# Kernel tuning notes

Hardware: AMD Instinct MI355X
Metric: run time of the kernel (lower is better)

## Reference

```python
import jax, jax.numpy as jnp
import numpy as np


def setup_inputs() -> dict:
    key = jax.random.key(0)
    ks = jax.random.split(key, 7)
    B, T, C, H = 8, 2048, 2048, 128
    x = jax.random.normal(ks[0], (B, T, C), dtype=jnp.float32)
    Wq = jax.random.normal(ks[1], (C, H), dtype=jnp.float32) * (C ** -0.5)
    bq = jax.random.normal(ks[2], (H,), dtype=jnp.float32) * 0.02
    Wk = jax.random.normal(ks[3], (C, H), dtype=jnp.float32) * (C ** -0.5)
    bk = jax.random.normal(ks[4], (H,), dtype=jnp.float32) * 0.02
    Wv = jax.random.normal(ks[5], (C, H), dtype=jnp.float32) * (C ** -0.5)
    bv = jax.random.normal(ks[6], (H,), dtype=jnp.float32) * 0.02
    return {"x": x, "Wq": Wq, "bq": bq, "Wk": Wk, "bk": bk, "Wv": Wv, "bv": bv}


def reference(x, Wq, bq, Wk, bk, Wv, bv):
    # Single-head causal self-attention (dropout in eval mode = identity).
    B, T, C = x.shape
    H = Wq.shape[1]
    Q = jnp.einsum("btc,ch->bth", x, Wq) + bq  # [B,T,H]
    K = jnp.einsum("btc,ch->bth", x, Wk) + bk
    V = jnp.einsum("btc,ch->bth", x, Wv) + bv
    scale = H ** -0.5
    wei = jnp.einsum("bth,bsh->bts", Q, K) * scale  # [B,T,T]
    causal = jnp.tril(jnp.ones((T, T), dtype=bool))
    wei = jnp.where(causal, wei, -jnp.inf)
    wei = jax.nn.softmax(wei, axis=-1)
    out = jnp.einsum("bts,bsh->bth", wei, V)  # [B,T,H]
    return out
```

## Files before the change

kernel.cpp:

```cpp
#include <hip/hip_runtime.h>

typedef float f32x4 __attribute__((ext_vector_type(4)));
typedef short short8 __attribute__((ext_vector_type(8)));
typedef unsigned short ushort8 __attribute__((ext_vector_type(8)));

#define AS1 __attribute__((address_space(1)))
#define AS3 __attribute__((address_space(3)))

#define WS_Q  786432
#define WS_K  2883584
#define WS_VT 4980736

__device__ __forceinline__ unsigned short f2bf(float x) {
    unsigned u = __float_as_uint(x);
    u += 0x7FFFu + ((u >> 16) & 1u);
    return (unsigned short)(u >> 16);
}

__device__ __forceinline__ short8 cvt8(float4 lo, float4 hi) {
    union { unsigned u[4]; short8 s; } r;
    asm("v_cvt_pk_bf16_f32 %0, %1, %2" : "=v"(r.u[0]) : "v"(lo.x), "v"(lo.y));
    asm("v_cvt_pk_bf16_f32 %0, %1, %2" : "=v"(r.u[1]) : "v"(lo.z), "v"(lo.w));
    asm("v_cvt_pk_bf16_f32 %0, %1, %2" : "=v"(r.u[2]) : "v"(hi.x), "v"(hi.y));
    asm("v_cvt_pk_bf16_f32 %0, %1, %2" : "=v"(r.u[3]) : "v"(hi.z), "v"(hi.w));
    return r.s;
}

__device__ __forceinline__ int swz128(int row, int cbyte) {
    return row * 128 + (cbyte ^ ((row & 7) << 4));
}

__global__ __launch_bounds__(256) void wt_kernel(const float* __restrict__ Wq,
        const float* __restrict__ Wk, const float* __restrict__ Wv,
        unsigned short* __restrict__ ws) {
    __shared__ __align__(16) unsigned short tile[64][136];
    int mat = blockIdx.x >> 5, ct = blockIdx.x & 31;
    const float* W = (mat == 0) ? Wq : ((mat == 1) ? Wk : Wv);
    int cbase = ct * 64;
    int tid = threadIdx.x;
#pragma unroll
    for (int p = 0; p < 8; p++) {
        int fidx = p * 256 + tid;
        int row = fidx >> 5;
        int c4 = (fidx & 31) << 2;
        float4 v = *(const float4*)&W[(size_t)(cbase + row) * 128 + c4];
        tile[row][c4 + 0] = f2bf(v.x);
        tile[row][c4 + 1] = f2bf(v.y);
        tile[row][c4 + 2] = f2bf(v.z);
        tile[row][c4 + 3] = f2bf(v.w);
    }
    __syncthreads();
    int h = tid >> 1, seg = tid & 1;
    unsigned short* base = ws + mat * 262144 + ct * 8192 + h * 64;
#pragma unroll
    for (int q4 = 0; q4 < 4; q4++) {
        ushort8 pk;
#pragma unroll
        for (int e = 0; e < 8; e++) pk[e] = tile[seg * 32 + q4 * 8 + e][h];
        int g = seg * 4 + q4;
        *(ushort8*)(base + ((g ^ (h & 7)) << 3)) = pk;
    }
}

__global__ __launch_bounds__(256, 3) void qkv_kernel(const float* __restrict__ x,
        const float* __restrict__ bq, const float* __restrict__ bk,
        const float* __restrict__ bv, unsigned short* __restrict__ ws) {
    __shared__ __align__(16) char lds[2][24576];
    int bid = blockIdx.x;
    int g = bid / 24, j = bid - g * 24;
    int matrix = j >> 3;
    int mt = g * 8 + (j & 7);
    const unsigned short* WTt = ws + matrix * 262144;
    const float* x0 = x + (size_t)mt * 64 * 2048;
    int tid = threadIdx.x, lane = tid & 63, wid = tid >> 6;
    int lr = lane & 15, lg = lane >> 4;
    int m0 = (wid >> 1) * 32, n0 = (wid & 1) * 64;

    int rowA = tid >> 2, qa = tid & 3;
    const float* aSrc = x0 + (size_t)rowA * 2048 + qa * 16;
    int aD0 = rowA * 128 + ((((qa * 2 + 0)) ^ (rowA & 7)) << 4);
    int aD1 = rowA * 128 + ((((qa * 2 + 1)) ^ (rowA & 7)) << 4);

    int aOff00, aOff01, aOff10, aOff11;
    int bOff00, bOff01, bOff10, bOff11, bOff20, bOff21, bOff30, bOff31;
    {
        int r0 = m0 + lr, r1 = m0 + 16 + lr;
        aOff00 = r0 * 128 + (((0 * 4 + lg) ^ (r0 & 7)) << 4);
        aOff01 = r0 * 128 + (((1 * 4 + lg) ^ (r0 & 7)) << 4);
        aOff10 = r1 * 128 + (((0 * 4 + lg) ^ (r1 & 7)) << 4);
        aOff11 = r1 * 128 + (((1 * 4 + lg) ^ (r1 & 7)) << 4);
        int h0 = n0 + lr, h1 = n0 + 16 + lr, h2 = n0 + 32 + lr, h3 = n0 + 48 + lr;
        bOff00 = 8192 + h0 * 128 + (((0 * 4 + lg) ^ (h0 & 7)) << 4);
        bOff01 = 8192 + h0 * 128 + (((1 * 4 + lg) ^ (h0 & 7)) << 4);
        bOff10 = 8192 + h1 * 128 + (((0 * 4 + lg) ^ (h1 & 7)) << 4);
        bOff11 = 8192 + h1 * 128 + (((1 * 4 + lg) ^ (h1 & 7)) << 4);
        bOff20 = 8192 + h2 * 128 + (((0 * 4 + lg) ^ (h2 & 7)) << 4);
        bOff21 = 8192 + h2 * 128 + (((1 * 4 + lg) ^ (h2 & 7)) << 4);
        bOff30 = 8192 + h3 * 128 + (((0 * 4 + lg) ^ (h3 & 7)) << 4);
        bOff31 = 8192 + h3 * 128 + (((1 * 4 + lg) ^ (h3 & 7)) << 4);
    }

    f32x4 acc[2][4];
#pragma unroll
    for (int i = 0; i < 2; i++)
#pragma unroll
        for (int j3 = 0; j3 < 4; j3++) acc[i][j3] = (f32x4){0.f, 0.f, 0.f, 0.f};
    float4 rA0, rA1, rA2, rA3;

#define ISSUE_AB(BUF, T) do { \
        const float* ap_ = aSrc + (size_t)(T) * 64; \
        rA0 = *(const float4*)ap_;        rA1 = *(const float4*)(ap_ + 4); \
        rA2 = *(const float4*)(ap_ + 8);  rA3 = *(const float4*)(ap_ + 12); \
        const unsigned short* bs_ = WTt + (size_t)(T) * 8192 + tid * 8; \
        char* bd_ = &lds[BUF][8192] + tid * 16; \
        __builtin_amdgcn_global_load_lds((const AS1 unsigned*)(bs_), \
            (AS3 unsigned*)(bd_), 16, 0, 0); \
        __builtin_amdgcn_global_load_lds((const AS1 unsigned*)(bs_ + 2048), \
            (AS3 unsigned*)(bd_ + 4096), 16, 0, 0); \
        __builtin_amdgcn_global_load_lds((const AS1 unsigned*)(bs_ + 4096), \
            (AS3 unsigned*)(bd_ + 8192), 16, 0, 0); \
        __builtin_amdgcn_global_load_lds((const AS1 unsigned*)(bs_ + 6144), \
            (AS3 unsigned*)(bd_ + 12288), 16, 0, 0); \
    } while (0)
#define WRITE_A(BUF) do { \
        short8 p0_ = cvt8(rA0, rA1); \
        short8 p1_ = cvt8(rA2, rA3); \
        *(short8*)(&lds[BUF][0] + aD0) = p0_; \
        *(short8*)(&lds[BUF][0] + aD1) = p1_; \
    } while (0)

#define QKV_BODY(T, CUR, STAGE, BAR) do { \
        if (STAGE) ISSUE_AB((CUR) ^ 1, (T) + 1); \
        const char* Lb_ = &lds[CUR][0]; \
        short8 a00 = *(const short8*)(Lb_ + aOff00); \
        short8 a01 = *(const short8*)(Lb_ + aOff01); \
        short8 a10 = *(const short8*)(Lb_ + aOff10); \
        short8 a11 = *(const short8*)(Lb_ + aOff11); \
        short8 b00 = *(const short8*)(Lb_ + bOff00); \
        short8 b01 = *(const short8*)(Lb_ + bOff01); \
        short8 b10 = *(const short8*)(Lb_ + bOff10); \
        short8 b11 = *(const short8*)(Lb_ + bOff11); \
        short8 b20 = *(const short8*)(Lb_ + bOff20); \
        short8 b21 = *(const short8*)(Lb_ + bOff21); \
        short8 b30 = *(const short8*)(Lb_ + bOff30); \
        short8 b31 = *(const short8*)(Lb_ + bOff31); \
        __builtin_amdgcn_s_setprio(1); \
        acc[0][0] = __builtin_amdgcn_mfma_f32_16x16x32_bf16(a00, b00, acc[0][0], 0, 0, 0); \
        acc[0][1] = __builtin_amdgcn_mfma_f32_16x16x32_bf16(a00, b10, acc[0][1], 0, 0, 0); \
        acc[0][2] = __builtin_amdgcn_mfma_f32_16x16x32_bf16(a00, b20, acc[0][2], 0, 0, 0); \
        acc[0][3] = __builtin_amdgcn_mfma_f32_16x16x32_bf16(a00, b30, acc[0][3], 0, 0, 0); \
        acc[1][0] = __builtin_amdgcn_mfma_f32_16x16x32_bf16(a10, b00, acc[1][0], 0, 0, 0); \
        acc[1][1] = __builtin_amdgcn_mfma_f32_16x16x32_bf16(a10, b10, acc[1][1], 0, 0, 0); \
        acc[1][2] = __builtin_amdgcn_mfma_f32_16x16x32_bf16(a10, b20, acc[1][2], 0, 0, 0); \
        acc[1][3] = __builtin_amdgcn_mfma_f32_16x16x32_bf16(a10, b30, acc[1][3], 0, 0, 0); \
        acc[0][0] = __builtin_amdgcn_mfma_f32_16x16x32_bf16(a01, b01, acc[0][0], 0, 0, 0); \
        acc[0][1] = __builtin_amdgcn_mfma_f32_16x16x32_bf16(a01, b11, acc[0][1], 0, 0, 0); \
        acc[0][2] = __builtin_amdgcn_mfma_f32_16x16x32_bf16(a01, b21, acc[0][2], 0, 0, 0); \
        acc[0][3] = __builtin_amdgcn_mfma_f32_16x16x32_bf16(a01, b31, acc[0][3], 0, 0, 0); \
        acc[1][0] = __builtin_amdgcn_mfma_f32_16x16x32_bf16(a11, b01, acc[1][0], 0, 0, 0); \
        acc[1][1] = __builtin_amdgcn_mfma_f32_16x16x32_bf16(a11, b11, acc[1][1], 0, 0, 0); \
        acc[1][2] = __builtin_amdgcn_mfma_f32_16x16x32_bf16(a11, b21, acc[1][2], 0, 0, 0); \
        acc[1][3] = __builtin_amdgcn_mfma_f32_16x16x32_bf16(a11, b31, acc[1][3], 0, 0, 0); \
        __builtin_amdgcn_s_setprio(0); \
        if (STAGE) { \
            asm volatile("s_waitcnt vmcnt(0)" ::: "memory"); \
            WRITE_A((CUR) ^ 1); \
            asm volatile("s_waitcnt lgkmcnt(0)" ::: "memory"); \
        } \
        if (BAR) __builtin_amdgcn_s_barrier(); \
    } while (0)

    ISSUE_AB(0, 0);
    asm volatile("s_waitcnt vmcnt(0)" ::: "memory");
    WRITE_A(0);
    asm volatile("s_waitcnt lgkmcnt(0)" ::: "memory");
    __builtin_amdgcn_s_barrier();

    for (int t2 = 0; t2 < 15; t2++) {
        int t = t2 * 2;
        QKV_BODY(t + 0, 0, true, true);
        QKV_BODY(t + 1, 1, true, true);
    }
    QKV_BODY(30, 0, true,  true);
    QKV_BODY(31, 1, false, false);

    const float* bias = (matrix == 0) ? bq : ((matrix == 1) ? bk : bv);
    float bb[4];
#pragma unroll
    for (int j3 = 0; j3 < 4; j3++) bb[j3] = bias[n0 + j3 * 16 + lr];
    if (matrix < 2) {
        unsigned short* outp = ws + ((matrix == 0) ? WS_Q : WS_K);
        float sc = (matrix == 0) ? 0.08838834764831845f : 1.0f;
#pragma unroll
        for (int i = 0; i < 2; i++)
#pragma unroll
            for (int j3 = 0; j3 < 4; j3++) {
                int h = n0 + j3 * 16 + lr;
#pragma unroll
                for (int r = 0; r < 4; r++) {
                    size_t t = (size_t)mt * 64 + m0 + i * 16 + (lg << 2) + r;
                    outp[t * 128 + h] = f2bf((acc[i][j3][r] + bb[j3]) * sc);
                }
            }
    } else {
        __syncthreads();
        unsigned short* sm = (unsigned short*)&lds[0][0];
#pragma unroll
        for (int i = 0; i < 2; i++)
#pragma unroll
            for (int j3 = 0; j3 < 4; j3++) {
                int h = n0 + j3 * 16 + lr;
#pragma unroll
                for (int r = 0; r < 4; r++) {
                    int tl = m0 + i * 16 + (lg << 2) + r;
                    sm[tl * 136 + h] = f2bf(acc[i][j3][r] + bb[j3]);
                }
            }
        __syncthreads();
        int h = tid & 127, seg = tid >> 7;
        int b2 = mt >> 5;
        int tin = (mt & 31) * 64 + seg * 32;
        unsigned short* vt = ws + WS_VT + ((size_t)b2 * 128 + h) * 2048 + tin;
#pragma unroll
        for (int q4 = 0; q4 < 4; q4++) {
            ushort8 pk;
#pragma unroll
            for (int e = 0; e < 8; e++) pk[e] = sm[(seg * 32 + q4 * 8 + e) * 136 + h];
            *(ushort8*)(vt + q4 * 8) = pk;
        }
    }
#undef QKV_BODY
#undef WRITE_A
#undef ISSUE_AB
}

__global__ __launch_bounds__(256, 2) void attn_kernel(const unsigned short* __restrict__ ws,
        float* __restrict__ out) {
    __shared__ __align__(16) float o_lds[4][32][128];
    __shared__ float ml[4][2][32];
    int b = blockIdx.x;
    int qi = 63 - (int)blockIdx.y;
    int qbase = qi * 32;
    int tid = threadIdx.x, lane = tid & 63, w = tid >> 6;
    int lr = lane & 15, lg = lane >> 4;
    const unsigned short* Qb = ws + WS_Q + (size_t)b * 2048 * 128;
    const unsigned short* Kb = ws + WS_K + (size_t)b * 2048 * 128;
    const unsigned short* Vt = ws + WS_VT + (size_t)b * 128 * 2048;
    char* p_lds = (char*)&o_lds[w][0][0];

    short8 qf[2][4];
#pragma unroll
    for (int i = 0; i < 2; i++)
#pragma unroll
        for (int kf = 0; kf < 4; kf++)
            qf[i][kf] = *(const short8*)&Qb[(size_t)(qbase + i * 16 + lr) * 128 + kf * 32 + lg * 8];

    f32x4 o[2][8];
#pragma unroll
    for (int i = 0; i < 2; i++)
#pragma unroll
        for (int jn = 0; jn < 8; jn++) o[i][jn] = (f32x4){0.f, 0.f, 0.f, 0.f};
    float mrow[2][4], lrow[2][4];
#pragma unroll
    for (int i = 0; i < 2; i++)
#pragma unroll
        for (int r = 0; r < 4; r++) { mrow[i][r] = -__builtin_inff(); lrow[i][r] = 0.f; }

    int ntiles = qi / 2 + 1;
    for (int ti = w; ti < ntiles; ti += 4) {
        int sb = ti * 64;
        f32x4 s[2][4];
#pragma unroll
        for (int i = 0; i < 2; i++)
#pragma unroll
            for (int nf = 0; nf < 4; nf++) s[i][nf] = (f32x4){0.f, 0.f, 0.f, 0.f};
        {
            short8 kb[4][4];
#pragma unroll
            for (int nf = 0; nf < 4; nf++)
#pragma unroll
                for (int kf = 0; kf < 4; kf++)
                    kb[nf][kf] = *(const short8*)&Kb[(size_t)(sb + nf * 16 + lr) * 128 + kf * 32 + lg * 8];
#pragma unroll
            for (int kf = 0; kf < 4; kf++)
#pragma unroll
                for (int i = 0; i < 2; i++)
#pragma unroll
                    for (int nf = 0; nf < 4; nf++)
                        s[i][nf] = __builtin_amdgcn_mfma_f32_16x16x32_bf16(qf[i][kf], kb[nf][kf], s[i][nf], 0, 0, 0);
        }
        if (sb + 63 > qbase) {
#pragma unroll
            for (int i = 0; i < 2; i++)
#pragma unroll
                for (int nf = 0; nf < 4; nf++)
#pragma unroll
                    for (int r = 0; r < 4; r++) {
                        int sg = sb + nf * 16 + lr;
                        int qg = qbase + i * 16 + (lg << 2) + r;
                        if (sg > qg) s[i][nf][r] = -__builtin_inff();
                    }
        }
        float alpha[2][4];
#pragma unroll
        for (int i = 0; i < 2; i++)
#pragma unroll
            for (int r = 0; r < 4; r++) {
                float pm = fmaxf(fmaxf(s[i][0][r], s[i][1][r]), fmaxf(s[i][2][r], s[i][3][r]));
                pm = fmaxf(pm, __shfl_xor(pm, 1));
                pm = fmaxf(pm, __shfl_xor(pm, 2));
                pm = fmaxf(pm, __shfl_xor(pm, 4));
                pm = fmaxf(pm, __shfl_xor(pm, 8));
                float mn = fmaxf(mrow[i][r], pm);
                alpha[i][r] = __expf(mrow[i][r] - mn);
                mrow[i][r] = mn;
            }
#pragma unroll
        for (int i = 0; i < 2; i++)
#pragma unroll
            for (int r = 0; r < 4; r++) {
                float rs = 0.f;
#pragma unroll
                for (int nf = 0; nf < 4; nf++) {
                    float p = __expf(s[i][nf][r] - mrow[i][r]);
                    s[i][nf][r] = p;
                    rs += p;
                }
                rs += __shfl_xor(rs, 1);
                rs += __shfl_xor(rs, 2);
                rs += __shfl_xor(rs, 4);
                rs += __shfl_xor(rs, 8);
                lrow[i][r] = lrow[i][r] * alpha[i][r] + rs;
            }
#pragma unroll
        for (int i = 0; i < 2; i++)
#pragma unroll
            for (int jn = 0; jn < 8; jn++)
#pragma unroll
                for (int r = 0; r < 4; r++) o[i][jn][r] *= alpha[i][r];
#pragma unroll
        for (int i = 0; i < 2; i++)
#pragma unroll
            for (int nf = 0; nf < 4; nf++)
#pragma unroll
                for (int r = 0; r < 4; r++) {
                    int row = i * 16 + (lg << 2) + r;
                    int cb2 = (nf * 16 + lr) * 2;
                    *(unsigned short*)(p_lds + swz128(row, cb2)) = f2bf(s[i][nf][r]);
                }
        asm volatile("s_waitcnt lgkmcnt(0)" ::: "memory");
        short8 pa[2][2];
#pragma unroll
        for (int i = 0; i < 2; i++)
#pragma unroll
            for (int kf = 0; kf < 2; kf++)
                pa[i][kf] = *(const short8*)(p_lds + swz128(i * 16 + lr, kf * 64 + lg * 16));
        short8 vb[8][2];
#pragma unroll
        for (int nf = 0; nf < 8; nf++)
#pragma unroll
            for (int kf = 0; kf < 2; kf++)
                vb[nf][kf] = *(const short8*)&Vt[(size_t)(nf * 16 + lr) * 2048 + sb + kf * 32 + lg * 8];
#pragma unroll
        for (int i = 0; i < 2; i++)
#pragma unroll
            for (int nf = 0; nf < 8; nf++)
#pragma unroll
                for (int kf = 0; kf < 2; kf++)
                    o[i][nf] = __builtin_amdgcn_mfma_f32_16x16x32_bf16(pa[i][kf], vb[nf][kf], o[i][nf], 0, 0, 0);
    }
#pragma unroll
    for (int i = 0; i < 2; i++)
#pragma unroll
        for (int r = 0; r < 4; r++) {
            int q = i * 16 + (lg << 2) + r;
            ml[w][0][q] = mrow[i][r];
            ml[w][1][q] = lrow[i][r];
        }
    asm volatile("s_waitcnt lgkmcnt(0)" ::: "memory");
#pragma unroll
    for (int i = 0; i < 2; i++)
#pragma unroll
        for (int jn = 0; jn < 8; jn++)
#pragma unroll
            for (int r = 0; r < 4; r++)
                o_lds[w][i * 16 + (lg << 2) + r][jn * 16 + lr] = o[i][jn][r];
    __syncthreads();
    int q = tid >> 3, h0 = (tid & 7) << 4;
    float mg = fmaxf(fmaxf(ml[0][0][q], ml[1][0][q]), fmaxf(ml[2][0][q], ml[3][0][q]));
    float scw[4], den = 0.f;
#pragma unroll
    for (int w4 = 0; w4 < 4; w4++) {
        scw[w4] = __expf(ml[w4][0][q] - mg);
        den += scw[w4] * ml[w4][1][q];
    }
    float inv = 1.0f / den;
    float* op = out + ((size_t)b * 2048 + qbase + q) * 128 + h0;
#pragma unroll
    for (int jj = 0; jj < 4; jj++) {
        f32x4 a4 = (f32x4){0.f, 0.f, 0.f, 0.f};
#pragma unroll
        for (int w4 = 0; w4 < 4; w4++) {
            f32x4 v = *(const f32x4*)&o_lds[w4][q][h0 + jj * 4];
            a4 += scw[w4] * v;
        }
        a4 *= inv;
        *(f32x4*)(op + jj * 4) = a4;
    }
}

extern "C" void kernel_launch(void* const* d_in, const int* in_sizes, int n_in,
                              void* d_out, int out_size, void* d_ws, size_t ws_size,
                              hipStream_t stream) {
    (void)in_sizes; (void)n_in; (void)out_size; (void)ws_size;
    const float* x  = (const float*)d_in[0];
    const float* Wq = (const float*)d_in[1];
    const float* bq = (const float*)d_in[2];
    const float* Wk = (const float*)d_in[3];
    const float* bk = (const float*)d_in[4];
    const float* Wv = (const float*)d_in[5];
    const float* bv = (const float*)d_in[6];
    unsigned short* ws = (unsigned short*)d_ws;
    float* out = (float*)d_out;

    wt_kernel<<<96, 256, 0, stream>>>(Wq, Wk, Wv, ws);
    qkv_kernel<<<768, 256, 0, stream>>>(x, bq, bk, bv, ws);
    attn_kernel<<<dim3(8, 64), 256, 0, stream>>>(ws, out);
}
```

Before: 113.2 us.

## Triple-buffer QKV GEMM with direct-to-LDS fp32 A loads and K=32 steps

```diff
diff --git a/kernel.cpp b/kernel.cpp
--- a/kernel.cpp
+++ b/kernel.cpp
@@ -51,21 +51,22 @@
     }
     __syncthreads();
     int h = tid >> 1, seg = tid & 1;
-    unsigned short* base = ws + mat * 262144 + ct * 8192 + h * 64;
-#pragma unroll
-    for (int q4 = 0; q4 < 4; q4++) {
+    int ks = ct * 2 + seg;
+    unsigned short* base = ws + mat * 262144 + ks * 4096 + h * 32;
+    int hx = (h >> 1) & 3;
+#pragma unroll
+    for (int u = 0; u < 4; u++) {
         ushort8 pk;
 #pragma unroll
-        for (int e = 0; e < 8; e++) pk[e] = tile[seg * 32 + q4 * 8 + e][h];
-        int g = seg * 4 + q4;
-        *(ushort8*)(base + ((g ^ (h & 7)) << 3)) = pk;
+        for (int e = 0; e < 8; e++) pk[e] = tile[seg * 32 + u * 8 + e][h];
+        *(ushort8*)(base + ((u ^ hx) << 3)) = pk;
     }
 }
 
 __global__ __launch_bounds__(256, 3) void qkv_kernel(const float* __restrict__ x,
         const float* __restrict__ bq, const float* __restrict__ bk,
         const float* __restrict__ bv, unsigned short* __restrict__ ws) {
-    __shared__ __align__(16) char lds[2][24576];
+    __shared__ __align__(16) char lds[3][16384];
     int bid = blockIdx.x;
     int g = bid / 24, j = bid - g * 24;
     int matrix = j >> 3;
@@ -76,28 +77,27 @@
     int lr = lane & 15, lg = lane >> 4;
     int m0 = (wid >> 1) * 32, n0 = (wid & 1) * 64;
 
-    int rowA = tid >> 2, qa = tid & 3;
-    const float* aSrc = x0 + (size_t)rowA * 2048 + qa * 16;
-    int aD0 = rowA * 128 + ((((qa * 2 + 0)) ^ (rowA & 7)) << 4);
-    int aD1 = rowA * 128 + ((((qa * 2 + 1)) ^ (rowA & 7)) << 4);
-
-    int aOff00, aOff01, aOff10, aOff11;
-    int bOff00, bOff01, bOff10, bOff11, bOff20, bOff21, bOff30, bOff31;
+    int rA = tid >> 3;
+    int pA = tid & 7;
+    int cA = pA ^ (rA & 7);
+    const float* aSrc0 = x0 + (size_t)rA * 2048 + cA * 4;
+    const float* aSrc1 = aSrc0 + (size_t)32 * 2048;
+    int aDst0 = tid * 16, aDst1 = tid * 16 + 4096;
+
+    int bDst0 = 8192 + tid * 16, bDst1 = 8192 + 4096 + tid * 16;
+
+    int aOff00, aOff01, aOff10, aOff11, bOff0, bOff1, bOff2, bOff3;
     {
         int r0 = m0 + lr, r1 = m0 + 16 + lr;
-        aOff00 = r0 * 128 + (((0 * 4 + lg) ^ (r0 & 7)) << 4);
-        aOff01 = r0 * 128 + (((1 * 4 + lg) ^ (r0 & 7)) << 4);
-        aOff10 = r1 * 128 + (((0 * 4 + lg) ^ (r1 & 7)) << 4);
-        aOff11 = r1 * 128 + (((1 * 4 + lg) ^ (r1 & 7)) << 4);
+        aOff00 = r0 * 128 + (((lg * 2 + 0) ^ (r0 & 7)) << 4);
+        aOff01 = r0 * 128 + (((lg * 2 + 1) ^ (r0 & 7)) << 4);
+        aOff10 = r1 * 128 + (((lg * 2 + 0) ^ (r1 & 7)) << 4);
+        aOff11 = r1 * 128 + (((lg * 2 + 1) ^ (r1 & 7)) << 4);
         int h0 = n0 + lr, h1 = n0 + 16 + lr, h2 = n0 + 32 + lr, h3 = n0 + 48 + lr;
-        bOff00 = 8192 + h0 * 128 + (((0 * 4 + lg) ^ (h0 & 7)) << 4);
-        bOff01 = 8192 + h0 * 128 + (((1 * 4 + lg) ^ (h0 & 7)) << 4);
-        bOff10 = 8192 + h1 * 128 + (((0 * 4 + lg) ^ (h1 & 7)) << 4);
-        bOff11 = 8192 + h1 * 128 + (((1 * 4 + lg) ^ (h1 & 7)) << 4);
-        bOff20 = 8192 + h2 * 128 + (((0 * 4 + lg) ^ (h2 & 7)) << 4);
-        bOff21 = 8192 + h2 * 128 + (((1 * 4 + lg) ^ (h2 & 7)) << 4);
-        bOff30 = 8192 + h3 * 128 + (((0 * 4 + lg) ^ (h3 & 7)) << 4);
-        bOff31 = 8192 + h3 * 128 + (((1 * 4 + lg) ^ (h3 & 7)) << 4);
+        bOff0 = 8192 + h0 * 64 + ((lg ^ ((h0 >> 1) & 3)) << 4);
+        bOff1 = 8192 + h1 * 64 + ((lg ^ ((h1 >> 1) & 3)) << 4);
+        bOff2 = 8192 + h2 * 64 + ((lg ^ ((h2 >> 1) & 3)) << 4);
+        bOff3 = 8192 + h3 * 64 + ((lg ^ ((h3 >> 1) & 3)) << 4);
     }
 
     f32x4 acc[2][4];
@@ -105,84 +105,71 @@
     for (int i = 0; i < 2; i++)
 #pragma unroll
         for (int j3 = 0; j3 < 4; j3++) acc[i][j3] = (f32x4){0.f, 0.f, 0.f, 0.f};
-    float4 rA0, rA1, rA2, rA3;
-
-#define ISSUE_AB(BUF, T) do { \
-        const float* ap_ = aSrc + (size_t)(T) * 64; \
-        rA0 = *(const float4*)ap_;        rA1 = *(const float4*)(ap_ + 4); \
-        rA2 = *(const float4*)(ap_ + 8);  rA3 = *(const float4*)(ap_ + 12); \
-        const unsigned short* bs_ = WTt + (size_t)(T) * 8192 + tid * 8; \
-        char* bd_ = &lds[BUF][8192] + tid * 16; \
-        __builtin_amdgcn_global_load_lds((const AS1 unsigned*)(bs_), \
-            (AS3 unsigned*)(bd_), 16, 0, 0); \
+
+#define ISSUE(BUF, T) do { \
+        char* Lb_ = &lds[BUF][0]; \
+        const float* a0_ = aSrc0 + (size_t)(T) * 32; \
+        const float* a1_ = aSrc1 + (size_t)(T) * 32; \
+        __builtin_amdgcn_global_load_lds((const AS1 unsigned*)a0_, \
+            (AS3 unsigned*)(Lb_ + aDst0), 16, 0, 0); \
+        __builtin_amdgcn_global_load_lds((const AS1 unsigned*)a1_, \
+            (AS3 unsigned*)(Lb_ + aDst1), 16, 0, 0); \
+        const unsigned short* bs_ = WTt + (size_t)(T) * 4096 + tid * 8; \
+        __builtin_amdgcn_global_load_lds((const AS1 unsigned*)bs_, \
+            (AS3 unsigned*)(Lb_ + bDst0), 16, 0, 0); \
         __builtin_amdgcn_global_load_lds((const AS1 unsigned*)(bs_ + 2048), \
-            (AS3 unsigned*)(bd_ + 4096), 16, 0, 0); \
-        __builtin_amdgcn_global_load_lds((const AS1 unsigned*)(bs_ + 4096), \
-            (AS3 unsigned*)(bd_ + 8192), 16, 0, 0); \
-        __builtin_amdgcn_global_load_lds((const AS1 unsigned*)(bs_ + 6144), \
-            (AS3 unsigned*)(bd_ + 12288), 16, 0, 0); \
+            (AS3 unsigned*)(Lb_ + bDst1), 16, 0, 0); \
     } while (0)
-#define WRITE_A(BUF) do { \
-        short8 p0_ = cvt8(rA0, rA1); \
-        short8 p1_ = cvt8(rA2, rA3); \
-        *(short8*)(&lds[BUF][0] + aD0) = p0_; \
-        *(short8*)(&lds[BUF][0] + aD1) = p1_; \
+
+#define BODY(U, T, STAGE, WAITN, BAR) do { \
+        if (STAGE) ISSUE(((U) + 2) % 3, (T) + 2); \
+        const char* Lb_ = &lds[U][0]; \
+        float4 alo0 = *(const float4*)(Lb_ + aOff00); \
+        float4 ahi0 = *(const float4*)(Lb_ + aOff01); \
+        float4 alo1 = *(const float4*)(Lb_ + aOff10); \
+        float4 ahi1 = *(const float4*)(Lb_ + aOff11); \
+        short8 b0 = *(const short8*)(Lb_ + bOff0); \
+        short8 b1 = *(const short8*)(Lb_ + bOff1); \
+        short8 b2 = *(const short8*)(Lb_ + bOff2); \
+        short8 b3 = *(const short8*)(Lb_ + bOff3); \
+        short8 a0 = cvt8(alo0, ahi0); \
+        short8 a1 = cvt8(alo1, ahi1); \
+        __builtin_amdgcn_s_setprio(1); \
+        acc[0][0] = __builtin_amdgcn_mfma_f32_16x16x32_bf16(a0, b0, acc[0][0], 0, 0, 0); \
+        acc[0][1] = __builtin_amdgcn_mfma_f32_16x16x32_bf16(a0, b1, acc[0][1], 0, 0, 0); \
+        acc[0][2] = __builtin_amdgcn_mfma_f32_16x16x32_bf16(a0, b2, acc[0][2], 0, 0, 0); \
+        acc[0][3] = __builtin_amdgcn_mfma_f32_16x16x32_bf16(a0, b3, acc[0][3], 0, 0, 0); \
+        acc[1][0] = __builtin_amdgcn_mfma_f32_16x16x32_bf16(a1, b0, acc[1][0], 0, 0, 0); \
+        acc[1][1] = __builtin_amdgcn_mfma_f32_16x16x32_bf16(a1, b1, acc[1][1], 0, 0, 0); \
+        acc[1][2] = __builtin_amdgcn_mfma_f32_16x16x32_bf16(a1, b2, acc[1][2], 0, 0, 0); \
+        acc[1][3] = __builtin_amdgcn_mfma_f32_16x16x32_bf16(a1, b3, acc[1][3], 0, 0, 0); \
+        __builtin_amdgcn_s_setprio(0); \
+        if ((WAITN) == 4)      { asm volatile("s_waitcnt vmcnt(4)" ::: "memory"); } \
+        else if ((WAITN) == 0) { asm volatile("s_waitcnt vmcnt(0)" ::: "memory"); } \
+        if (BAR) { \
+            __builtin_amdgcn_s_barrier(); \
+            asm volatile("" ::: "memory");    \
+        } \
     } while (0)
 
-#define QKV_BODY(T, CUR, STAGE, BAR) do { \
-        if (STAGE) ISSUE_AB((CUR) ^ 1, (T) + 1); \
-        const char* Lb_ = &lds[CUR][0]; \
-        short8 a00 = *(const short8*)(Lb_ + aOff00); \
-        short8 a01 = *(const short8*)(Lb_ + aOff01); \
-        short8 a10 = *(const short8*)(Lb_ + aOff10); \
-        short8 a11 = *(const short8*)(Lb_ + aOff11); \
-        short8 b00 = *(const short8*)(Lb_ + bOff00); \
-        short8 b01 = *(const short8*)(Lb_ + bOff01); \
-        short8 b10 = *(const short8*)(Lb_ + bOff10); \
-        short8 b11 = *(const short8*)(Lb_ + bOff11); \
-        short8 b20 = *(const short8*)(Lb_ + bOff20); \
-        short8 b21 = *(const short8*)(Lb_ + bOff21); \
-        short8 b30 = *(const short8*)(Lb_ + bOff30); \
-        short8 b31 = *(const short8*)(Lb_ + bOff31); \
-        __builtin_amdgcn_s_setprio(1); \
-        acc[0][0] = __builtin_amdgcn_mfma_f32_16x16x32_bf16(a00, b00, acc[0][0], 0, 0, 0); \
-        acc[0][1] = __builtin_amdgcn_mfma_f32_16x16x32_bf16(a00, b10, acc[0][1], 0, 0, 0); \
-        acc[0][2] = __builtin_amdgcn_mfma_f32_16x16x32_bf16(a00, b20, acc[0][2], 0, 0, 0); \
-        acc[0][3] = __builtin_amdgcn_mfma_f32_16x16x32_bf16(a00, b30, acc[0][3], 0, 0, 0); \
-        acc[1][0] = __builtin_amdgcn_mfma_f32_16x16x32_bf16(a10, b00, acc[1][0], 0, 0, 0); \
-        acc[1][1] = __builtin_amdgcn_mfma_f32_16x16x32_bf16(a10, b10, acc[1][1], 0, 0, 0); \
-        acc[1][2] = __builtin_amdgcn_mfma_f32_16x16x32_bf16(a10, b20, acc[1][2], 0, 0, 0); \
-        acc[1][3] = __builtin_amdgcn_mfma_f32_16x16x32_bf16(a10, b30, acc[1][3], 0, 0, 0); \
-        acc[0][0] = __builtin_amdgcn_mfma_f32_16x16x32_bf16(a01, b01, acc[0][0], 0, 0, 0); \
-        acc[0][1] = __builtin_amdgcn_mfma_f32_16x16x32_bf16(a01, b11, acc[0][1], 0, 0, 0); \
-        acc[0][2] = __builtin_amdgcn_mfma_f32_16x16x32_bf16(a01, b21, acc[0][2], 0, 0, 0); \
-        acc[0][3] = __builtin_amdgcn_mfma_f32_16x16x32_bf16(a01, b31, acc[0][3], 0, 0, 0); \
-        acc[1][0] = __builtin_amdgcn_mfma_f32_16x16x32_bf16(a11, b01, acc[1][0], 0, 0, 0); \
-        acc[1][1] = __builtin_amdgcn_mfma_f32_16x16x32_bf16(a11, b11, acc[1][1], 0, 0, 0); \
-        acc[1][2] = __builtin_amdgcn_mfma_f32_16x16x32_bf16(a11, b21, acc[1][2], 0, 0, 0); \
-        acc[1][3] = __builtin_amdgcn_mfma_f32_16x16x32_bf16(a11, b31, acc[1][3], 0, 0, 0); \
-        __builtin_amdgcn_s_setprio(0); \
-        if (STAGE) { \
-            asm volatile("s_waitcnt vmcnt(0)" ::: "memory"); \
-            WRITE_A((CUR) ^ 1); \
-            asm volatile("s_waitcnt lgkmcnt(0)" ::: "memory"); \
-        } \
-        if (BAR) __builtin_amdgcn_s_barrier(); \
-    } while (0)
-
-    ISSUE_AB(0, 0);
-    asm volatile("s_waitcnt vmcnt(0)" ::: "memory");
-    WRITE_A(0);
-    asm volatile("s_waitcnt lgkmcnt(0)" ::: "memory");
+    ISSUE(0, 0);
+    ISSUE(1, 1);
+    asm volatile("s_waitcnt vmcnt(4)" ::: "memory");
     __builtin_amdgcn_s_barrier();
-
-    for (int t2 = 0; t2 < 15; t2++) {
-        int t = t2 * 2;
-        QKV_BODY(t + 0, 0, true, true);
-        QKV_BODY(t + 1, 1, true, true);
-    }
-    QKV_BODY(30, 0, true,  true);
-    QKV_BODY(31, 1, false, false);
+    asm volatile("" ::: "memory");
+
+    for (int t3 = 0; t3 < 20; t3++) {
+        int T0 = t3 * 3;
+        BODY(0, T0 + 0, true, 4, true);
+        BODY(1, T0 + 1, true, 4, true);
+        BODY(2, T0 + 2, true, 4, true);
+    }
+    BODY(0, 60, true,  4,  true);
+    BODY(1, 61, true,  4,  true);
+    BODY(2, 62, false, 0,  true);
+    BODY(0, 63, false, -1, false);
+#undef BODY
+#undef ISSUE
 
     const float* bias = (matrix == 0) ? bq : ((matrix == 1) ? bk : bv);
     float bb[4];
@@ -229,9 +216,6 @@
             *(ushort8*)(vt + q4 * 8) = pk;
         }
     }
-#undef QKV_BODY
-#undef WRITE_A
-#undef ISSUE_AB
 }
 
 __global__ __launch_bounds__(256, 2) void attn_kernel(const unsigned short* __restrict__ ws,
```

New measurement: 110.8 us. 1.02x faster.
